# Kernel tuning notes

Measured on AMD Instinct MI355X. Metric: run time of the kernel, lower is better.

The kernel has to match this reference:

```python
import jax, jax.numpy as jnp
import numpy as np

N_NODES = 50000
N_EDGES = 800000
IN_DIM = 128
HID_DIM = 64
OUT_DIM = 64
NUM_GRAPHS = 512


def setup_inputs() -> dict:
    key = jax.random.key(0)
    ks = jax.random.split(key, 8)
    x = jax.random.normal(ks[0], (N_NODES, IN_DIM), dtype=jnp.float32)
    edge_index = jax.random.randint(ks[1], (2, N_EDGES), 0, N_NODES, dtype=jnp.int64)
    batch = jnp.sort(jax.random.randint(ks[2], (N_NODES,), 0, NUM_GRAPHS, dtype=jnp.int64))
    s1 = 1.0 / np.sqrt(IN_DIM)
    s2 = 1.0 / np.sqrt(HID_DIM)
    W1 = jax.random.uniform(ks[3], (IN_DIM, HID_DIM), jnp.float32, -s1, s1)
    b1 = jax.random.uniform(ks[4], (HID_DIM,), jnp.float32, -s1, s1)
    W2 = jax.random.uniform(ks[5], (HID_DIM, OUT_DIM), jnp.float32, -s2, s2)
    b2 = jax.random.uniform(ks[6], (OUT_DIM,), jnp.float32, -s2, s2)
    return {"x": x, "edge_index": edge_index, "batch": batch,
            "W1": W1, "b1": b1, "W2": W2, "b2": b2}


def _gcn_layer(h, W, b, src, dst, norm, n_nodes):
    # linear transform first (keeps the per-edge gather at output width)
    h = h @ W + b                      # [N, d_out]
    msg = h[src] * norm[:, None]       # [E, d_out] gathered, normalized messages
    agg = jax.ops.segment_sum(msg, dst, num_segments=n_nodes)  # scatter-add
    return jax.nn.relu(agg)


def reference(x, edge_index, batch, W1, b1, W2, b2):
    src, dst = edge_index[0], edge_index[1]
    # symmetric degree normalization: deg^{-1/2}[src] * deg^{-1/2}[dst]
    deg = jax.ops.segment_sum(jnp.ones((src.shape[0],), x.dtype), dst,
                              num_segments=N_NODES)
    dinv = jax.lax.rsqrt(jnp.maximum(deg, 1.0))
    norm = dinv[src] * dinv[dst]       # [E]

    h = _gcn_layer(x, W1, b1, src, dst, norm, N_NODES)   # dropout = identity (eval)
    h = _gcn_layer(h, W2, b2, src, dst, norm, N_NODES)

    # scatter_mean pooling over batch indices
    sums = jax.ops.segment_sum(h, batch, num_segments=NUM_GRAPHS)
    cnts = jax.ops.segment_sum(jnp.ones((N_NODES,), h.dtype), batch,
                               num_segments=NUM_GRAPHS)
    return sums / jnp.maximum(cnts, 1.0)[:, None]        # [NUM_GRAPHS, OUT_DIM]
```

## Files before the change

### kernel.cpp

```cpp
#include <hip/hip_runtime.h>
#include <hip/hip_fp16.h>

#define N_NODES 50000
#define N_EDGES 800000
#define IN_DIM 128
#define HID_DIM 64
#define OUT_DIM 64
#define NUM_GRAPHS 512
#define CAP 64
#define NB 196
#define BCAP 5120
#define FILL_T 2048
#define NFILL ((N_EDGES + FILL_T - 1) / FILL_T)
#define GEMM_BLKS ((N_NODES + 31) / 32)

typedef unsigned short u16;
typedef unsigned int u32;

__global__ __launch_bounds__(256) void gemm1_fill_kernel(
    const float* __restrict__ X, const float* __restrict__ W,
    const float* __restrict__ bias, __half* __restrict__ Yh, int n_nodes,
    const int* __restrict__ src, const int* __restrict__ dst,
    int* __restrict__ gcursor, u32* __restrict__ packed, int n_edges) {
    __shared__ float xs[32][IN_DIM];
    __shared__ int hist[256], cnt2[256], goffs[256];
    const int tid = threadIdx.x;

    if (blockIdx.x & 1) {
        const int fb = blockIdx.x >> 1;
        if (fb >= NFILL) return;
        hist[tid] = 0; cnt2[tid] = 0;
        __syncthreads();
        const int base = fb * FILL_T;
        int d[8], s[8];
#pragma unroll
        for (int i = 0; i < 8; ++i) {
            int e = base + i * 256 + tid;
            if (e < n_edges) {
                d[i] = dst[e]; s[i] = src[e];
                atomicAdd(&hist[d[i] >> 8], 1);
            } else d[i] = -1;
        }
        __syncthreads();
        if (hist[tid] > 0) goffs[tid] = atomicAdd(&gcursor[tid], hist[tid]);
        __syncthreads();
#pragma unroll
        for (int i = 0; i < 8; ++i) {
            if (d[i] >= 0) {
                int b = d[i] >> 8;
                int p = goffs[b] + atomicAdd(&cnt2[b], 1);
                packed[(size_t)b * BCAP + p] = ((u32)d[i] << 16) | (u32)s[i];
            }
        }
        return;
    }

    const int idx = blockIdx.x >> 1;
    if (idx >= GEMM_BLKS) return;
    const int base = idx * 32;
    const int nvec = 32 * IN_DIM / 4;
    const float4* X4 = reinterpret_cast<const float4*>(X + (size_t)base * IN_DIM);
    float4* xs4 = reinterpret_cast<float4*>(&xs[0][0]);
    for (int i = tid; i < nvec; i += 256) {
        int row = i / (IN_DIM / 4);
        xs4[i] = (base + row < n_nodes) ? X4[i] : make_float4(0.f, 0.f, 0.f, 0.f);
    }
    __syncthreads();

    const int j = tid & 63;
    const int w = tid >> 6;
    float b = bias[j];
    float c[8];
#pragma unroll
    for (int r = 0; r < 8; ++r) c[r] = b;
#pragma unroll 4
    for (int k = 0; k < IN_DIM; ++k) {
        float wv = W[k * 64 + j];
#pragma unroll
        for (int r = 0; r < 8; ++r) c[r] += wv * xs[w * 8 + r][k];
    }
    int n0 = base + w * 8;
#pragma unroll
    for (int r = 0; r < 8; ++r)
        if (n0 + r < n_nodes)
            Yh[(size_t)(n0 + r) * 64 + j] = __float2half(c[r]);
}

__global__ __launch_bounds__(256) void fine_kernel(
    const u32* __restrict__ packed, const int* __restrict__ gcursor,
    u16* __restrict__ ssorted, int* __restrict__ deg, float* __restrict__ dinv,
    __half* __restrict__ H1h,
    const int* __restrict__ batch, int* __restrict__ gstart, int n_graphs) {
    __shared__ u16 image[128 * CAP];
    __shared__ int cur[128];
    __shared__ float ds[128];
    const int tid = threadIdx.x;

    if (blockIdx.x == 2 * NB) {
        for (int g = tid; g <= n_graphs; g += 256) {
            int lo = 0, hi = N_NODES;
            while (lo < hi) {
                int mid = (lo + hi) >> 1;
                if (batch[mid] < g) lo = mid + 1; else hi = mid;
            }
            gstart[g] = lo;
        }
        return;
    }

    const int b = blockIdx.x >> 1;
    const int half = blockIdx.x & 1;
    if (tid < 128) cur[tid] = 0;
    __syncthreads();
    const int cnt = gcursor[b];
    const u32* pp = packed + (size_t)b * BCAP;
    for (int i = tid; i < cnt; i += 256) {
        u32 p = pp[i];
        int dl = (p >> 16) & 255;
        if ((dl >> 7) == half) {
            int loc = dl & 127;
            int pos = atomicAdd(&cur[loc], 1);
            if (pos < CAP) image[loc * CAP + pos] = (u16)(p & 0xffff);
        }
    }
    __syncthreads();
    const int nbase = b * 256 + half * 128;
    if (tid < 128) {
        int c = cur[tid];
        float dv = rsqrtf(fmaxf((float)c, 1.0f));
        ds[tid] = dv;
        int d = nbase + tid;
        if (d < N_NODES) { deg[d] = c; dinv[d] = dv; }
    }
    __syncthreads();
    const u32* im32 = reinterpret_cast<const u32*>(image);
    u32* out32 = reinterpret_cast<u32*>(ssorted) + (size_t)nbase * (CAP / 2);
    for (int i = tid; i < 128 * CAP / 2; i += 256) out32[i] = im32[i];
    __half2* H2 = reinterpret_cast<__half2*>(H1h) + (size_t)nbase * 32;
    const int lim = min(128, N_NODES - nbase) * 32;
    for (int i = tid; i < lim; i += 256) {
        float dv = ds[i >> 5];
        float2 f = __half22float2(H2[i]);
        H2[i] = __floats2half2_rn(f.x * dv, f.y * dv);
    }
}

__device__ __forceinline__ void acc_row(const uint4& v, float2& aa, float2& ab,
                                        float2& ac, float2& ad) {
    const __half2* hp = reinterpret_cast<const __half2*>(&v);
    float2 f;
    f = __half22float2(hp[0]); aa.x += f.x; aa.y += f.y;
    f = __half22float2(hp[1]); ab.x += f.x; ab.y += f.y;
    f = __half22float2(hp[2]); ac.x += f.x; ac.y += f.y;
    f = __half22float2(hp[3]); ad.x += f.x; ad.y += f.y;
}

__global__ __launch_bounds__(256) void agg_gemm_kernel(
    const __half* __restrict__ H, const u16* __restrict__ ssorted,
    const int* __restrict__ deg, const float* __restrict__ dinv,
    const float* __restrict__ W, const float* __restrict__ bias,
    __half* __restrict__ Yh, int n_nodes) {
    __shared__ float xs[32][64];
    const int tid = threadIdx.x;
    const int lane = tid & 63;
    const int w = tid >> 6;
    const int lo = lane & 7;
    const int slot = w * 8 + (lane >> 3);
    const int base = blockIdx.x * 32;
    const uint4* H16 = reinterpret_cast<const uint4*>(H);

    int node = base + slot;
    float2 aa = make_float2(0.f, 0.f), ab = make_float2(0.f, 0.f);
    float2 ac = make_float2(0.f, 0.f), ad = make_float2(0.f, 0.f);
    if (node < n_nodes) {
        int dg = min(deg[node], CAP);
        const u16* sp = ssorted + (size_t)node * CAP;
        int i = 0;
        for (; i + 3 < dg; i += 4) {
            ushort4 s4 = *reinterpret_cast<const ushort4*>(sp + i);
            uint4 v0 = H16[(size_t)s4.x * 8 + lo];
            uint4 v1 = H16[(size_t)s4.y * 8 + lo];
            uint4 v2 = H16[(size_t)s4.z * 8 + lo];
            uint4 v3 = H16[(size_t)s4.w * 8 + lo];
            acc_row(v0, aa, ab, ac, ad);
            acc_row(v1, aa, ab, ac, ad);
            acc_row(v2, aa, ab, ac, ad);
            acc_row(v3, aa, ab, ac, ad);
        }
        for (; i < dg; ++i) {
            uint4 v = H16[(size_t)sp[i] * 8 + lo];
            acc_row(v, aa, ab, ac, ad);
        }
        float dv = dinv[node];
        *reinterpret_cast<float4*>(&xs[slot][8 * lo]) =
            make_float4(fmaxf(aa.x * dv, 0.f), fmaxf(aa.y * dv, 0.f),
                        fmaxf(ab.x * dv, 0.f), fmaxf(ab.y * dv, 0.f));
        *reinterpret_cast<float4*>(&xs[slot][8 * lo + 4]) =
            make_float4(fmaxf(ac.x * dv, 0.f), fmaxf(ac.y * dv, 0.f),
                        fmaxf(ad.x * dv, 0.f), fmaxf(ad.y * dv, 0.f));
    } else {
        *reinterpret_cast<float4*>(&xs[slot][8 * lo]) = make_float4(0.f, 0.f, 0.f, 0.f);
        *reinterpret_cast<float4*>(&xs[slot][8 * lo + 4]) = make_float4(0.f, 0.f, 0.f, 0.f);
    }
    __syncthreads();

    float b = bias[lane];
    float c[8];
#pragma unroll
    for (int r = 0; r < 8; ++r) c[r] = b;
#pragma unroll 4
    for (int k = 0; k < 64; ++k) {
        float wv = W[k * 64 + lane];
#pragma unroll
        for (int r = 0; r < 8; ++r) c[r] += wv * xs[w * 8 + r][k];
    }
    int n0 = base + w * 8;
#pragma unroll
    for (int r = 0; r < 8; ++r)
        if (n0 + r < n_nodes)
            Yh[(size_t)(n0 + r) * 64 + lane] = __float2half(c[r] * dinv[n0 + r]);
}

__global__ __launch_bounds__(512) void agg2_pool_kernel(
    const __half* __restrict__ H, const u16* __restrict__ ssorted,
    const int* __restrict__ deg, const float* __restrict__ dinv,
    const int* __restrict__ gstart, float* __restrict__ out) {
    __shared__ float part[64][64];
    const int g = blockIdx.x;
    const int tid = threadIdx.x;
    const int lane = tid & 63;
    const int w = tid >> 6;
    const int lo = lane & 7;
    const int slot = w * 8 + (lane >> 3);
    const uint4* H16 = reinterpret_cast<const uint4*>(H);
    const int beg = gstart[g], end = gstart[g + 1];

    float2 pa = make_float2(0.f, 0.f), pb = make_float2(0.f, 0.f);
    float2 pc = make_float2(0.f, 0.f), pd = make_float2(0.f, 0.f);
    for (int node = beg + slot; node < end; node += 64) {
        int dg = min(deg[node], CAP);
        const u16* sp = ssorted + (size_t)node * CAP;
        float2 aa = make_float2(0.f, 0.f), ab = make_float2(0.f, 0.f);
        float2 ac = make_float2(0.f, 0.f), ad = make_float2(0.f, 0.f);
        int i = 0;
        for (; i + 3 < dg; i += 4) {
            ushort4 s4 = *reinterpret_cast<const ushort4*>(sp + i);
            uint4 v0 = H16[(size_t)s4.x * 8 + lo];
            uint4 v1 = H16[(size_t)s4.y * 8 + lo];
            uint4 v2 = H16[(size_t)s4.z * 8 + lo];
            uint4 v3 = H16[(size_t)s4.w * 8 + lo];
            acc_row(v0, aa, ab, ac, ad);
            acc_row(v1, aa, ab, ac, ad);
            acc_row(v2, aa, ab, ac, ad);
            acc_row(v3, aa, ab, ac, ad);
        }
        for (; i < dg; ++i) {
            uint4 v = H16[(size_t)sp[i] * 8 + lo];
            acc_row(v, aa, ab, ac, ad);
        }
        float dv = dinv[node];
        pa.x += fmaxf(aa.x * dv, 0.f); pa.y += fmaxf(aa.y * dv, 0.f);
        pb.x += fmaxf(ab.x * dv, 0.f); pb.y += fmaxf(ab.y * dv, 0.f);
        pc.x += fmaxf(ac.x * dv, 0.f); pc.y += fmaxf(ac.y * dv, 0.f);
        pd.x += fmaxf(ad.x * dv, 0.f); pd.y += fmaxf(ad.y * dv, 0.f);
    }
    *reinterpret_cast<float4*>(&part[slot][8 * lo]) = make_float4(pa.x, pa.y, pb.x, pb.y);
    *reinterpret_cast<float4*>(&part[slot][8 * lo + 4]) = make_float4(pc.x, pc.y, pd.x, pd.y);
    __syncthreads();
    if (tid < 64) {
        float s = 0.f;
#pragma unroll
        for (int r = 0; r < 64; ++r) s += part[r][tid];
        out[(size_t)g * 64 + tid] = s / fmaxf((float)(end - beg), 1.0f);
    }
}

extern "C" void kernel_launch(void* const* d_in, const int* in_sizes, int n_in,
                              void* d_out, int out_size, void* d_ws, size_t ws_size,
                              hipStream_t stream) {
    const float* x     = (const float*)d_in[0];
    const int*   ei    = (const int*)d_in[1];
    const int*   batch = (const int*)d_in[2];
    const float* W1    = (const float*)d_in[3];
    const float* b1    = (const float*)d_in[4];
    const float* W2    = (const float*)d_in[5];
    const float* b2    = (const float*)d_in[6];
    float* out = (float*)d_out;

    const int* srcp = ei;
    const int* dstp = ei + N_EDGES;

    __half* H1h     = (__half*)d_ws;
    __half* H2h     = H1h + (size_t)N_NODES * 64;
    float*  dinv    = (float*)(H2h + (size_t)N_NODES * 64);
    int*    deg     = (int*)(dinv + N_NODES);
    u16*    ssorted = (u16*)(deg + N_NODES);
    u32*    packed  = (u32*)(ssorted + (size_t)NB * 256 * CAP);
    int*    gcursor = (int*)(packed + (size_t)NB * BCAP);
    int*    gstart  = gcursor + 256;

    hipMemsetAsync(gcursor, 0, 256 * sizeof(int), stream);

    gemm1_fill_kernel<<<2 * GEMM_BLKS, 256, 0, stream>>>(
        x, W1, b1, H1h, N_NODES, srcp, dstp, gcursor, packed, N_EDGES);

    fine_kernel<<<2 * NB + 1, 256, 0, stream>>>(
        packed, gcursor, ssorted, deg, dinv, H1h, batch, gstart, NUM_GRAPHS);

    agg_gemm_kernel<<<(N_NODES + 31) / 32, 256, 0, stream>>>(
        H1h, ssorted, deg, dinv, W2, b2, H2h, N_NODES);

    agg2_pool_kernel<<<NUM_GRAPHS, 512, 0, stream>>>(
        H2h, ssorted, deg, dinv, gstart, out);
}
```

Before: 173.3 us.

## Fuse all GCN stages into one persistent cooperative kernel with grid syncs

Replaces the memset plus four separate kernel launches with a single cooperative persistent kernel. Blocks loop over tiles for each stage (fill+gemm1, fine bucketing, agg+gemm2, agg+pool) and are separated by grid.sync(). This targets launch overhead and inter-kernel gaps. In exchange it adds grid-wide barrier costs and limits occupancy to the cooperative grid size, and the pool stage now runs with 256 threads per graph instead of 512. The original multi-kernel path remains as a fallback.

```diff
diff --git a/kernel.cpp b/kernel.cpp
--- a/kernel.cpp
+++ b/kernel.cpp
@@ -1,21 +1,282 @@
 #include <hip/hip_runtime.h>
 #include <hip/hip_fp16.h>
+#include <hip/hip_cooperative_groups.h>
+
+namespace cg = cooperative_groups;
 
 #define N_NODES 50000
 #define N_EDGES 800000
 #define IN_DIM 128
-#define HID_DIM 64
-#define OUT_DIM 64
 #define NUM_GRAPHS 512
 #define CAP 64
 #define NB 196
 #define BCAP 5120
 #define FILL_T 2048
-#define NFILL ((N_EDGES + FILL_T - 1) / FILL_T)
-#define GEMM_BLKS ((N_NODES + 31) / 32)
+#define NFILL 391
+#define GEMM_TILES 1563
 
 typedef unsigned short u16;
 typedef unsigned int u32;
+
+__device__ __forceinline__ void acc_row(const uint4& v, float2& aa, float2& ab,
+                                        float2& ac, float2& ad) {
+    const __half2* hp = reinterpret_cast<const __half2*>(&v);
+    float2 f;
+    f = __half22float2(hp[0]); aa.x += f.x; aa.y += f.y;
+    f = __half22float2(hp[1]); ab.x += f.x; ab.y += f.y;
+    f = __half22float2(hp[2]); ac.x += f.x; ac.y += f.y;
+    f = __half22float2(hp[3]); ad.x += f.x; ad.y += f.y;
+}
+
+__global__ __launch_bounds__(256, 4) void mega_kernel(
+    const float* __restrict__ X, const int* __restrict__ src,
+    const int* __restrict__ dst, const int* __restrict__ batch,
+    const float* __restrict__ W1, const float* __restrict__ b1,
+    const float* __restrict__ W2, const float* __restrict__ b2,
+    float* __restrict__ out,
+    __half* __restrict__ H1h, __half* __restrict__ H2h,
+    float* __restrict__ dinv, int* __restrict__ deg,
+    u16* __restrict__ ssorted, u32* __restrict__ packed,
+    int* __restrict__ gcursor, int* __restrict__ gstart) {
+    __shared__ __align__(16) unsigned char smem[20480];
+    cg::grid_group grid = cg::this_grid();
+    const int tid = threadIdx.x;
+    const int bid = blockIdx.x;
+    const int nblk = gridDim.x;
+
+    if (bid == 0) gcursor[tid] = 0;
+    grid.sync();
+
+    for (int t = bid; t < NFILL + GEMM_TILES; t += nblk) {
+        __syncthreads();
+        if (t < NFILL) {
+            int* hist = (int*)smem;
+            int* cnt2 = hist + 256;
+            int* goffs = cnt2 + 256;
+            hist[tid] = 0; cnt2[tid] = 0;
+            __syncthreads();
+            const int base = t * FILL_T;
+            int d[8], s[8];
+#pragma unroll
+            for (int i = 0; i < 8; ++i) {
+                int e = base + i * 256 + tid;
+                if (e < N_EDGES) {
+                    d[i] = dst[e]; s[i] = src[e];
+                    atomicAdd(&hist[d[i] >> 8], 1);
+                } else d[i] = -1;
+            }
+            __syncthreads();
+            if (hist[tid] > 0) goffs[tid] = atomicAdd(&gcursor[tid], hist[tid]);
+            __syncthreads();
+#pragma unroll
+            for (int i = 0; i < 8; ++i) {
+                if (d[i] >= 0) {
+                    int b = d[i] >> 8;
+                    int p = goffs[b] + atomicAdd(&cnt2[b], 1);
+                    packed[(size_t)b * BCAP + p] = ((u32)d[i] << 16) | (u32)s[i];
+                }
+            }
+        } else {
+            const int idx = t - NFILL;
+            float (*xs)[IN_DIM] = reinterpret_cast<float(*)[IN_DIM]>(smem);
+            const int nb = idx * 32;
+            const int nvec = 32 * IN_DIM / 4;
+            const float4* X4 = reinterpret_cast<const float4*>(X + (size_t)nb * IN_DIM);
+            float4* xs4 = reinterpret_cast<float4*>(&xs[0][0]);
+            for (int i = tid; i < nvec; i += 256) {
+                int row = i / (IN_DIM / 4);
+                xs4[i] = (nb + row < N_NODES) ? X4[i] : make_float4(0.f, 0.f, 0.f, 0.f);
+            }
+            __syncthreads();
+            const int j = tid & 63;
+            const int w = tid >> 6;
+            float bb = b1[j];
+            float c[8];
+#pragma unroll
+            for (int r = 0; r < 8; ++r) c[r] = bb;
+#pragma unroll 4
+            for (int k = 0; k < IN_DIM; ++k) {
+                float wv = W1[k * 64 + j];
+#pragma unroll
+                for (int r = 0; r < 8; ++r) c[r] += wv * xs[w * 8 + r][k];
+            }
+            int n0 = nb + w * 8;
+#pragma unroll
+            for (int r = 0; r < 8; ++r)
+                if (n0 + r < N_NODES)
+                    H1h[(size_t)(n0 + r) * 64 + j] = __float2half(c[r]);
+        }
+    }
+    grid.sync();
+
+    for (int v = bid; v < 2 * NB + 1; v += nblk) {
+        __syncthreads();
+        if (v == 2 * NB) {
+            for (int g = tid; g <= NUM_GRAPHS; g += 256) {
+                int lo = 0, hi = N_NODES;
+                while (lo < hi) {
+                    int mid = (lo + hi) >> 1;
+                    if (batch[mid] < g) lo = mid + 1; else hi = mid;
+                }
+                gstart[g] = lo;
+            }
+            continue;
+        }
+        const int b = v >> 1;
+        const int half = v & 1;
+        u16* image = (u16*)smem;
+        int* cur = (int*)(smem + 16384);
+        float* ds = (float*)(smem + 16896);
+        if (tid < 128) cur[tid] = 0;
+        __syncthreads();
+        const int cnt = gcursor[b];
+        const u32* pp = packed + (size_t)b * BCAP;
+        for (int i = tid; i < cnt; i += 256) {
+            u32 p = pp[i];
+            int dl = (p >> 16) & 255;
+            if ((dl >> 7) == half) {
+                int loc = dl & 127;
+                int pos = atomicAdd(&cur[loc], 1);
+                if (pos < CAP) image[loc * CAP + pos] = (u16)(p & 0xffff);
+            }
+        }
+        __syncthreads();
+        const int nbase = b * 256 + half * 128;
+        if (tid < 128) {
+            int c = cur[tid];
+            float dv = rsqrtf(fmaxf((float)c, 1.0f));
+            ds[tid] = dv;
+            int d = nbase + tid;
+            if (d < N_NODES) { deg[d] = c; dinv[d] = dv; }
+        }
+        __syncthreads();
+        const u32* im32 = reinterpret_cast<const u32*>(image);
+        u32* out32 = reinterpret_cast<u32*>(ssorted) + (size_t)nbase * (CAP / 2);
+        for (int i = tid; i < 128 * CAP / 2; i += 256) out32[i] = im32[i];
+        __half2* Hp = reinterpret_cast<__half2*>(H1h) + (size_t)nbase * 32;
+        const int lim = min(128, N_NODES - nbase) * 32;
+        for (int i = tid; i < lim; i += 256) {
+            float dv = ds[i >> 5];
+            float2 f = __half22float2(Hp[i]);
+            Hp[i] = __floats2half2_rn(f.x * dv, f.y * dv);
+        }
+    }
+    grid.sync();
+
+    {
+        float (*xs)[64] = reinterpret_cast<float(*)[64]>(smem);
+        const int lane = tid & 63;
+        const int w = tid >> 6;
+        const int lo = lane & 7;
+        const int slot = w * 8 + (lane >> 3);
+        const uint4* H16 = reinterpret_cast<const uint4*>(H1h);
+        for (int t = bid; t < GEMM_TILES; t += nblk) {
+            __syncthreads();
+            const int nb = t * 32;
+            const int node = nb + slot;
+            float2 aa = make_float2(0.f, 0.f), ab = make_float2(0.f, 0.f);
+            float2 ac = make_float2(0.f, 0.f), ad = make_float2(0.f, 0.f);
+            if (node < N_NODES) {
+                int dg = min(deg[node], CAP);
+                const u16* sp = ssorted + (size_t)node * CAP;
+                int i = 0;
+                for (; i + 3 < dg; i += 4) {
+                    ushort4 s4 = *reinterpret_cast<const ushort4*>(sp + i);
+                    uint4 v0 = H16[(size_t)s4.x * 8 + lo];
+                    uint4 v1 = H16[(size_t)s4.y * 8 + lo];
+                    uint4 v2 = H16[(size_t)s4.z * 8 + lo];
+                    uint4 v3 = H16[(size_t)s4.w * 8 + lo];
+                    acc_row(v0, aa, ab, ac, ad);
+                    acc_row(v1, aa, ab, ac, ad);
+                    acc_row(v2, aa, ab, ac, ad);
+                    acc_row(v3, aa, ab, ac, ad);
+                }
+                for (; i < dg; ++i) {
+                    uint4 v = H16[(size_t)sp[i] * 8 + lo];
+                    acc_row(v, aa, ab, ac, ad);
+                }
+                float dv = dinv[node];
+                *reinterpret_cast<float4*>(&xs[slot][8 * lo]) =
+                    make_float4(fmaxf(aa.x * dv, 0.f), fmaxf(aa.y * dv, 0.f),
+                                fmaxf(ab.x * dv, 0.f), fmaxf(ab.y * dv, 0.f));
+                *reinterpret_cast<float4*>(&xs[slot][8 * lo + 4]) =
+                    make_float4(fmaxf(ac.x * dv, 0.f), fmaxf(ac.y * dv, 0.f),
+                                fmaxf(ad.x * dv, 0.f), fmaxf(ad.y * dv, 0.f));
+            } else {
+                *reinterpret_cast<float4*>(&xs[slot][8 * lo]) = make_float4(0.f, 0.f, 0.f, 0.f);
+                *reinterpret_cast<float4*>(&xs[slot][8 * lo + 4]) = make_float4(0.f, 0.f, 0.f, 0.f);
+            }
+            __syncthreads();
+            float bb = b2[lane];
+            float c[8];
+#pragma unroll
+            for (int r = 0; r < 8; ++r) c[r] = bb;
+#pragma unroll 4
+            for (int k = 0; k < 64; ++k) {
+                float wv = W2[k * 64 + lane];
+#pragma unroll
+                for (int r = 0; r < 8; ++r) c[r] += wv * xs[w * 8 + r][k];
+            }
+            int n0 = nb + w * 8;
+#pragma unroll
+            for (int r = 0; r < 8; ++r)
+                if (n0 + r < N_NODES)
+                    H2h[(size_t)(n0 + r) * 64 + lane] = __float2half(c[r] * dinv[n0 + r]);
+        }
+    }
+    grid.sync();
+
+    {
+        float (*part)[64] = reinterpret_cast<float(*)[64]>(smem);
+        const int lane = tid & 63;
+        const int w = tid >> 6;
+        const int lo = lane & 7;
+        const int slot = w * 8 + (lane >> 3);
+        const uint4* H16 = reinterpret_cast<const uint4*>(H2h);
+        for (int g = bid; g < NUM_GRAPHS; g += nblk) {
+            __syncthreads();
+            const int beg = gstart[g], end = gstart[g + 1];
+            float2 pa = make_float2(0.f, 0.f), pb = make_float2(0.f, 0.f);
+            float2 pc = make_float2(0.f, 0.f), pd = make_float2(0.f, 0.f);
+            for (int node = beg + slot; node < end; node += 32) {
+                int dg = min(deg[node], CAP);
+                const u16* sp = ssorted + (size_t)node * CAP;
+                float2 aa = make_float2(0.f, 0.f), ab = make_float2(0.f, 0.f);
+                float2 ac = make_float2(0.f, 0.f), ad = make_float2(0.f, 0.f);
+                int i = 0;
+                for (; i + 3 < dg; i += 4) {
+                    ushort4 s4 = *reinterpret_cast<const ushort4*>(sp + i);
+                    uint4 v0 = H16[(size_t)s4.x * 8 + lo];
+                    uint4 v1 = H16[(size_t)s4.y * 8 + lo];
+                    uint4 v2 = H16[(size_t)s4.z * 8 + lo];
+                    uint4 v3 = H16[(size_t)s4.w * 8 + lo];
+                    acc_row(v0, aa, ab, ac, ad);
+                    acc_row(v1, aa, ab, ac, ad);
+                    acc_row(v2, aa, ab, ac, ad);
+                    acc_row(v3, aa, ab, ac, ad);
+                }
+                for (; i < dg; ++i) {
+                    uint4 v = H16[(size_t)sp[i] * 8 + lo];
+                    acc_row(v, aa, ab, ac, ad);
+                }
+                float dv = dinv[node];
+                pa.x += fmaxf(aa.x * dv, 0.f); pa.y += fmaxf(aa.y * dv, 0.f);
+                pb.x += fmaxf(ab.x * dv, 0.f); pb.y += fmaxf(ab.y * dv, 0.f);
+                pc.x += fmaxf(ac.x * dv, 0.f); pc.y += fmaxf(ac.y * dv, 0.f);
+                pd.x += fmaxf(ad.x * dv, 0.f); pd.y += fmaxf(ad.y * dv, 0.f);
+            }
+            *reinterpret_cast<float4*>(&part[slot][8 * lo]) = make_float4(pa.x, pa.y, pb.x, pb.y);
+            *reinterpret_cast<float4*>(&part[slot][8 * lo + 4]) = make_float4(pc.x, pc.y, pd.x, pd.y);
+            __syncthreads();
+            if (tid < 64) {
+                float s = 0.f;
+#pragma unroll
+                for (int r = 0; r < 32; ++r) s += part[r][tid];
+                out[(size_t)g * 64 + tid] = s / fmaxf((float)(end - beg), 1.0f);
+            }
+        }
+    }
+}
 
 __global__ __launch_bounds__(256) void gemm1_fill_kernel(
     const float* __restrict__ X, const float* __restrict__ W,
@@ -25,7 +286,6 @@
     __shared__ float xs[32][IN_DIM];
     __shared__ int hist[256], cnt2[256], goffs[256];
     const int tid = threadIdx.x;
-
     if (blockIdx.x & 1) {
         const int fb = blockIdx.x >> 1;
         if (fb >= NFILL) return;
@@ -54,9 +314,8 @@
         }
         return;
     }
-
     const int idx = blockIdx.x >> 1;
-    if (idx >= GEMM_BLKS) return;
+    if (idx >= GEMM_TILES) return;
     const int base = idx * 32;
     const int nvec = 32 * IN_DIM / 4;
     const float4* X4 = reinterpret_cast<const float4*>(X + (size_t)base * IN_DIM);
@@ -66,7 +325,6 @@
         xs4[i] = (base + row < n_nodes) ? X4[i] : make_float4(0.f, 0.f, 0.f, 0.f);
     }
     __syncthreads();
-
     const int j = tid & 63;
     const int w = tid >> 6;
     float b = bias[j];
@@ -95,7 +353,6 @@
     __shared__ int cur[128];
     __shared__ float ds[128];
     const int tid = threadIdx.x;
-
     if (blockIdx.x == 2 * NB) {
         for (int g = tid; g <= n_graphs; g += 256) {
             int lo = 0, hi = N_NODES;
@@ -107,7 +364,6 @@
         }
         return;
     }
-
     const int b = blockIdx.x >> 1;
     const int half = blockIdx.x & 1;
     if (tid < 128) cur[tid] = 0;
@@ -136,23 +392,13 @@
     const u32* im32 = reinterpret_cast<const u32*>(image);
     u32* out32 = reinterpret_cast<u32*>(ssorted) + (size_t)nbase * (CAP / 2);
     for (int i = tid; i < 128 * CAP / 2; i += 256) out32[i] = im32[i];
-    __half2* H2 = reinterpret_cast<__half2*>(H1h) + (size_t)nbase * 32;
+    __half2* Hp = reinterpret_cast<__half2*>(H1h) + (size_t)nbase * 32;
     const int lim = min(128, N_NODES - nbase) * 32;
     for (int i = tid; i < lim; i += 256) {
         float dv = ds[i >> 5];
-        float2 f = __half22float2(H2[i]);
-        H2[i] = __floats2half2_rn(f.x * dv, f.y * dv);
-    }
-}
-
-__device__ __forceinline__ void acc_row(const uint4& v, float2& aa, float2& ab,
-                                        float2& ac, float2& ad) {
-    const __half2* hp = reinterpret_cast<const __half2*>(&v);
-    float2 f;
-    f = __half22float2(hp[0]); aa.x += f.x; aa.y += f.y;
-    f = __half22float2(hp[1]); ab.x += f.x; ab.y += f.y;
-    f = __half22float2(hp[2]); ac.x += f.x; ac.y += f.y;
-    f = __half22float2(hp[3]); ad.x += f.x; ad.y += f.y;
+        float2 f = __half22float2(Hp[i]);
+        Hp[i] = __floats2half2_rn(f.x * dv, f.y * dv);
+    }
 }
 
 __global__ __launch_bounds__(256) void agg_gemm_kernel(
@@ -168,7 +414,6 @@
     const int slot = w * 8 + (lane >> 3);
     const int base = blockIdx.x * 32;
     const uint4* H16 = reinterpret_cast<const uint4*>(H);
-
     int node = base + slot;
     float2 aa = make_float2(0.f, 0.f), ab = make_float2(0.f, 0.f);
     float2 ac = make_float2(0.f, 0.f), ad = make_float2(0.f, 0.f);
@@ -203,7 +448,6 @@
         *reinterpret_cast<float4*>(&xs[slot][8 * lo + 4]) = make_float4(0.f, 0.f, 0.f, 0.f);
     }
     __syncthreads();
-
     float b = bias[lane];
     float c[8];
 #pragma unroll
@@ -234,7 +478,6 @@
     const int slot = w * 8 + (lane >> 3);
     const uint4* H16 = reinterpret_cast<const uint4*>(H);
     const int beg = gstart[g], end = gstart[g + 1];
-
     float2 pa = make_float2(0.f, 0.f), pb = make_float2(0.f, 0.f);
     float2 pc = make_float2(0.f, 0.f), pd = make_float2(0.f, 0.f);
     for (int node = beg + slot; node < end; node += 64) {
@@ -299,17 +542,33 @@
     int*    gcursor = (int*)(packed + (size_t)NB * BCAP);
     int*    gstart  = gcursor + 256;
 
+    int maxBlocksPerCU = 0, numCU = 0, dev = 0;
+    hipError_t occ_err = hipOccupancyMaxActiveBlocksPerMultiprocessor(
+        &maxBlocksPerCU, mega_kernel, 256, 0);
+    hipGetDevice(&dev);
+    hipDeviceGetAttribute(&numCU, hipDeviceAttributeMultiprocessorCount, dev);
+    bool coop_ok = false;
+    if (occ_err == hipSuccess && maxBlocksPerCU > 0 && numCU > 0) {
+        int nblk = maxBlocksPerCU * numCU;
+        if (nblk > 2048) nblk = 2048;
+        void* args[] = {
+            (void*)&x, (void*)&srcp, (void*)&dstp, (void*)&batch,
+            (void*)&W1, (void*)&b1, (void*)&W2, (void*)&b2, (void*)&out,
+            (void*)&H1h, (void*)&H2h, (void*)&dinv, (void*)&deg,
+            (void*)&ssorted, (void*)&packed, (void*)&gcursor, (void*)&gstart};
+        hipError_t e = hipLaunchCooperativeKernel((void*)mega_kernel, dim3(nblk),
+                                                  dim3(256), args, 0, stream);
+        coop_ok = (e == hipSuccess);
+    }
+    if (coop_ok) return;
+
     hipMemsetAsync(gcursor, 0, 256 * sizeof(int), stream);
-
-    gemm1_fill_kernel<<<2 * GEMM_BLKS, 256, 0, stream>>>(
+    gemm1_fill_kernel<<<2 * GEMM_TILES, 256, 0, stream>>>(
         x, W1, b1, H1h, N_NODES, srcp, dstp, gcursor, packed, N_EDGES);
-
     fine_kernel<<<2 * NB + 1, 256, 0, stream>>>(
         packed, gcursor, ssorted, deg, dinv, H1h, batch, gstart, NUM_GRAPHS);
-
-    agg_gemm_kernel<<<(N_NODES + 31) / 32, 256, 0, stream>>>(
+    agg_gemm_kernel<<<GEMM_TILES, 256, 0, stream>>>(
         H1h, ssorted, deg, dinv, W2, b2, H2h, N_NODES);
-
     agg2_pool_kernel<<<NUM_GRAPHS, 512, 0, stream>>>(
         H2h, ssorted, deg, dinv, gstart, out);
 }
```

After: 500.2 us. +188.5%, slower.
